# Kernel optimization log

Measured on AMD Instinct MI355X. Metric: run time of the kernel, lower is better.

The kernel has to match this reference:

```python
import jax, jax.numpy as jnp
import numpy as np

EPS = 0.1  # residual scale from __init__


def setup_inputs() -> dict:
    key = jax.random.key(0)
    ks = jax.random.split(key, 13)
    T, B, E = 8, 4096, 16          # terms, batch(queries), predicates(edges)
    F = 1024                        # feature_dim = 2*emb_dim (emb_dim=512)
    M = 2 * F + 2                   # message_dim = 4*emb_dim + 2 = 2050
    H = 4096                        # hidden_dim

    def lin(k, fan_in, shape):
        return jax.random.normal(k, shape, jnp.float32) / np.sqrt(fan_in)

    return {
        "term_emb": jax.random.normal(ks[0], (T, B, F), jnp.float32),
        "pred_emb": jax.random.normal(ks[1], (E, B, F), jnp.float32),
        "W1": lin(ks[2], M, (M, H)),
        "b1": jnp.zeros((H,), jnp.float32),
        "W2": lin(ks[3], H, (H, F)),
        "b2": jnp.zeros((F,), jnp.float32),
        "M1": lin(ks[4], F, (F, H)),
        "mb1": jnp.zeros((H,), jnp.float32),
        "M2": lin(ks[5], H, (H, F)),
        "mb2": jnp.zeros((F,), jnp.float32),
        "head_idx": jax.random.randint(ks[6], (E,), 0, T, jnp.int32),
        "tail_idx": jax.random.randint(ks[7], (E,), 0, T, jnp.int32),
        "sign_bits": jax.random.randint(ks[8], (E,), 0, 2, jnp.int32),
    }


def reference(term_emb, pred_emb, W1, b1, W2, b2, M1, mb1, M2, mb2,
              head_idx, tail_idx, sign_bits):
    # term_emb: [T,B,F], pred_emb: [E,B,F]
    T = term_emb.shape[0]
    E, B, F = pred_emb.shape
    dt = pred_emb.dtype

    sign = (1.0 - 2.0 * sign_bits.astype(dt))[:, None, None]   # [E,1,1], +-1
    ones = jnp.ones((E, B, 1), dt)
    s_ones = sign * ones                                        # [E,B,1]

    h = term_emb[head_idx]                                      # gather [E,B,F]
    t = term_emb[tail_idx]                                      # gather [E,B,F]

    # message to head: [head_emb, pred_emb, +1, sign]
    # message to tail: [tail_emb, pred_emb, -1, sign]
    msg_h = jnp.concatenate([h, pred_emb, ones, s_ones], axis=-1)   # [E,B,M]
    msg_t = jnp.concatenate([t, pred_emb, -ones, s_ones], axis=-1)  # [E,B,M]

    msgs = jnp.concatenate([msg_h, msg_t], axis=0)              # [2E,B,M]
    seg = jnp.concatenate([head_idx, tail_idx], axis=0)         # [2E]
    agg = jax.ops.segment_sum(msgs, seg, num_segments=T)        # [T,B,M]

    # encoder MLP + eps residual
    enc = jax.nn.relu(agg @ W1 + b1) @ W2 + b2                  # [T,B,F]
    x = enc + EPS * term_emb

    # update MLP (layers == 1)
    out = jax.nn.relu(x @ M1 + mb1) @ M2 + mb2                  # [T,B,F]
    return out
```

## Files before the change

kernel.cpp:

```cpp
#include <hip/hip_runtime.h>
#include <hip/hip_bf16.h>
#include <cstdint>

typedef unsigned short u16;
typedef __attribute__((ext_vector_type(8))) u16 u16x8;
typedef __attribute__((ext_vector_type(8))) short s16x8;
typedef __attribute__((ext_vector_type(4))) float f32x4;

#define AS1(p) ((const __attribute__((address_space(1))) void*)(p))
#define AS3(p) ((__attribute__((address_space(3))) void*)(p))

__device__ __forceinline__ u16 f2bf(float f){
  union{float f; uint32_t i;} x; x.f = f;
  uint32_t r = x.i + 0x7fff + ((x.i>>16)&1);
  return (u16)(r>>16);
}

__global__ void transpose_f32_bf16(const float* __restrict__ in, u16* __restrict__ out,
                                   int K, int N){
  __shared__ u16 tile[32][33];
  const int tid = threadIdx.x;
  const int bx = blockIdx.x, by = blockIdx.y;
  const int xl = tid & 31, yl = tid >> 5;
  #pragma unroll
  for (int r = 0; r < 4; ++r){
    int y = by*32 + yl + r*8;
    tile[yl + r*8][xl] = f2bf(in[(size_t)y*N + bx*32 + xl]);
  }
  __syncthreads();
  #pragma unroll
  for (int r = 0; r < 4; ++r){
    int oy = bx*32 + yl + r*8;
    int ox = by*32 + xl;
    out[(size_t)oy*K + ox] = tile[xl][yl + r*8];
  }
}

__global__ void build_bias1(const float* __restrict__ W1, const float* __restrict__ b1,
                            const int* __restrict__ head, const int* __restrict__ tail,
                            const int* __restrict__ sign, float* __restrict__ bias1){
  int idx = blockIdx.x*256 + threadIdx.x;
  int t = idx >> 12, h = idx & 4095;
  float cH = 0.f, cS = 0.f;
  #pragma unroll
  for (int e = 0; e < 16; ++e){
    float s = 1.f - 2.f*(float)sign[e];
    if (head[e] == t){ cH += 1.f; cS += s; }
    if (tail[e] == t){ cH -= 1.f; cS += s; }
  }
  bias1[idx] = b1[h] + cH*W1[(size_t)2048*4096 + h] + cS*W1[(size_t)2049*4096 + h];
}

__global__ void build_x1(const float* __restrict__ term, const float* __restrict__ pred,
                         const int* __restrict__ head, const int* __restrict__ tail,
                         u16* __restrict__ X1, int r0){
  int idx = blockIdx.x*256 + threadIdx.x;
  int lr = idx >> 8;
  int c8 = (idx & 255) * 8;
  int grow = r0 + lr;
  int t = grow >> 12;
  int b = grow & 4095;
  float v[8];
  if (c8 < 1024){
    int deg = 0;
    #pragma unroll
    for (int e = 0; e < 16; ++e) deg += (head[e]==t) + (tail[e]==t);
    float d = (float)deg;
    const float4* p = (const float4*)(term + (size_t)grow*1024 + c8);
    float4 lo = p[0], hi = p[1];
    v[0]=d*lo.x; v[1]=d*lo.y; v[2]=d*lo.z; v[3]=d*lo.w;
    v[4]=d*hi.x; v[5]=d*hi.y; v[6]=d*hi.z; v[7]=d*hi.w;
  } else {
    int f = c8 - 1024;
    #pragma unroll
    for (int j = 0; j < 8; ++j) v[j] = 0.f;
    #pragma unroll
    for (int e = 0; e < 16; ++e){
      int w = (head[e]==t) + (tail[e]==t);
      if (w){
        const float4* p = (const float4*)(pred + ((size_t)e<<22) + ((size_t)b<<10) + f);
        float4 lo = p[0], hi = p[1];
        float fw = (float)w;
        v[0]+=fw*lo.x; v[1]+=fw*lo.y; v[2]+=fw*lo.z; v[3]+=fw*lo.w;
        v[4]+=fw*hi.x; v[5]+=fw*hi.y; v[6]+=fw*hi.z; v[7]+=fw*hi.w;
      }
    }
  }
  u16x8 o;
  #pragma unroll
  for (int j = 0; j < 8; ++j) o[j] = f2bf(v[j]);
  *(u16x8*)(X1 + (size_t)lr*2048 + c8) = o;
}

#define FENCE() asm volatile("" ::: "memory")
#define BAR()   do{ FENCE(); __builtin_amdgcn_s_barrier(); FENCE(); }while(0)
#define LGKM0() do{ asm volatile("s_waitcnt lgkmcnt(0)" ::: "memory"); \
                    __builtin_amdgcn_sched_barrier(0); }while(0)
#define VM6()   asm volatile("s_waitcnt vmcnt(6)" ::: "memory")

#define STAGE(isB, slot, half, kt) do{ \
    const u16* _s = (isB ? bStage : aStage) + ((half) ? halfStride : (size_t)0) + ((size_t)(kt) << 6); \
    u16* _d = &LDS[(isB ? 32768 : 0) + (slot)*16384 + (half)*8192 + tid*8]; \
    __builtin_amdgcn_global_load_lds(AS1(_s), AS3(_d), 16, 0, 0); \
    __builtin_amdgcn_global_load_lds(AS1(_s + q2s), AS3(_d + 4096), 16, 0, 0); \
  }while(0)

#define LOADA(slot, rh) do{ \
    _Pragma("unroll") \
    for (int ii = 0; ii < 4; ++ii){ \
      af[ii][0] = *(const s16x8*)&LDS[(slot)*16384 + aB + ((rh)*4+ii)*1024 + xv0]; \
      af[ii][1] = *(const s16x8*)&LDS[(slot)*16384 + aB + ((rh)*4+ii)*1024 + xv1]; \
    } }while(0)

#define LOADB(slot) do{ \
    _Pragma("unroll") \
    for (int jj = 0; jj < 4; ++jj){ \
      bfr[jj][0] = *(const s16x8*)&LDS[32768 + (slot)*16384 + bB + jj*1024 + xv0]; \
      bfr[jj][1] = *(const s16x8*)&LDS[32768 + (slot)*16384 + bB + jj*1024 + xv1]; \
    } }while(0)

#define MFMAQ(rh, ch) do{ \
    _Pragma("unroll") \
    for (int ii = 0; ii < 4; ++ii){ \
      _Pragma("unroll") \
      for (int jj = 0; jj < 2; ++jj){ \
        acc[(rh)*4+ii][(ch)*2+jj] = __builtin_amdgcn_mfma_f32_16x16x32_bf16(af[ii][0], bfr[(ch)*2+jj][0], acc[(rh)*4+ii][(ch)*2+jj], 0,0,0); \
        acc[(rh)*4+ii][(ch)*2+jj] = __builtin_amdgcn_mfma_f32_16x16x32_bf16(af[ii][1], bfr[(ch)*2+jj][1], acc[(rh)*4+ii][(ch)*2+jj], 0,0,0); \
      } } }while(0)

template<int MODE>
__launch_bounds__(512, 2)
__global__ void gemm256(const u16* __restrict__ A, const u16* __restrict__ Bt,
                        void* __restrict__ Cv, int N, int K, int r0,
                        const float* __restrict__ bias_mat,
                        const float* __restrict__ bias_vec,
                        const float* __restrict__ resid){
  __shared__ u16 LDS[65536];
  const int tid = threadIdx.x;
  const int lane = tid & 63;
  const int wid = tid >> 6;
  const int wr = wid >> 2, wc = wid & 3;
  const int frow = lane & 15, fgrp = lane >> 4;

  int nwg = gridDim.x * gridDim.y;
  int orig = blockIdx.y * gridDim.x + blockIdx.x;
  int id = orig;
  if ((nwg & 7) == 0){ int cpx = nwg >> 3; id = (orig & 7) * cpx + (orig >> 3); }
  const int bx = id % gridDim.x, by = id / gridDim.x;
  const int row0 = by * 256, col0 = bx * 256;

  const size_t rowK = (size_t)(tid >> 3) * K;
  const int sg8 = (((tid & 7) ^ ((tid >> 3) & 7)) << 3);
  const u16* aStage = A  + (size_t)row0 * K + rowK + sg8;
  const u16* bStage = Bt + (size_t)col0 * K + rowK + sg8;
  const size_t halfStride = (size_t)128 * K;
  const size_t q2s = (size_t)64 * K;

  const int xv0 = ((fgrp)     ^ (frow & 7)) << 3;
  const int xv1 = ((4 + fgrp) ^ (frow & 7)) << 3;
  const int aB = wr * 8192 + frow * 64;
  const int bB = (wc >> 1) * 8192 + (wc & 1) * 4096 + frow * 64;

  f32x4 acc[8][4];
  #pragma unroll
  for (int i = 0; i < 8; ++i)
    #pragma unroll
    for (int j = 0; j < 4; ++j) acc[i][j] = (f32x4){0.f,0.f,0.f,0.f};
  s16x8 af[4][2], bfr[4][2];

  const int NT = K >> 6;
  const int NI = NT >> 1;

  STAGE(1,0,0,0); STAGE(1,0,1,0); STAGE(0,0,0,0); STAGE(0,0,1,0);
  STAGE(1,1,0,1); STAGE(1,1,1,1); STAGE(0,1,0,1);
  VM6(); BAR();

  for (int i = 0; i < NI; ++i){
    const int kt1  = 2*i + 1;
    const int kn0  = (2*i + 2 < NT) ? 2*i + 2 : NT - 2;
    const int kn1  = (2*i + 3 < NT) ? 2*i + 3 : NT - 1;
    LOADA(0,0); LOADB(0);
    STAGE(0,1,1,kt1);
    BAR(); LGKM0();
    __builtin_amdgcn_s_setprio(1); MFMAQ(0,0); __builtin_amdgcn_s_setprio(0);
    BAR();
    STAGE(1,0,0,kn0);
    BAR();
    __builtin_amdgcn_s_setprio(1); MFMAQ(0,1); __builtin_amdgcn_s_setprio(0);
    BAR();
    LOADA(0,1);
    STAGE(1,0,1,kn0);
    BAR(); LGKM0();
    __builtin_amdgcn_s_setprio(1); MFMAQ(1,0); __builtin_amdgcn_s_setprio(0);
    BAR();
    STAGE(0,0,0,kn0);
    BAR();
    __builtin_amdgcn_s_setprio(1); MFMAQ(1,1); __builtin_amdgcn_s_setprio(0);
    VM6(); BAR();
    LOADA(1,0); LOADB(1);
    STAGE(0,0,1,kn0);
    BAR(); LGKM0();
    __builtin_amdgcn_s_setprio(1); MFMAQ(0,0); __builtin_amdgcn_s_setprio(0);
    BAR();
    STAGE(1,1,0,kn1);
    BAR();
    __builtin_amdgcn_s_setprio(1); MFMAQ(0,1); __builtin_amdgcn_s_setprio(0);
    BAR();
    LOADA(1,1);
    STAGE(1,1,1,kn1);
    BAR(); LGKM0();
    __builtin_amdgcn_s_setprio(1); MFMAQ(1,0); __builtin_amdgcn_s_setprio(0);
    BAR();
    STAGE(0,1,0,kn1);
    BAR();
    __builtin_amdgcn_s_setprio(1); MFMAQ(1,1); __builtin_amdgcn_s_setprio(0);
    VM6(); BAR();
  }

  #pragma unroll
  for (int i2 = 0; i2 < 8; ++i2){
    #pragma unroll
    for (int j2 = 0; j2 < 4; ++j2){
      #pragma unroll
      for (int r = 0; r < 4; ++r){
        int lrow = row0 + wr*128 + i2*16 + fgrp*4 + r;
        int col  = col0 + wc*64 + j2*16 + frow;
        float v = acc[i2][j2][r];
        if (MODE == 0){
          int grow = r0 + lrow;
          v += bias_mat[(size_t)(grow >> 12)*N + col];
          v = fmaxf(v, 0.f);
          ((u16*)Cv)[(size_t)lrow*N + col] = f2bf(v);
        } else if (MODE == 1){
          int grow = r0 + lrow;
          v += bias_vec[col] + 0.1f*resid[(size_t)grow*1024 + col];
          ((u16*)Cv)[(size_t)lrow*N + col] = f2bf(v);
        } else if (MODE == 2){
          v += bias_vec[col];
          v = fmaxf(v, 0.f);
          ((u16*)Cv)[(size_t)lrow*N + col] = f2bf(v);
        } else {
          v += bias_vec[col];
          ((float*)Cv)[(size_t)lrow*N + col] = v;
        }
      }
    }
  }
}

extern "C" void kernel_launch(void* const* d_in, const int* in_sizes, int n_in,
                              void* d_out, int out_size, void* d_ws, size_t ws_size,
                              hipStream_t stream){
  const float* term = (const float*)d_in[0];
  const float* pred = (const float*)d_in[1];
  const float* W1   = (const float*)d_in[2];
  const float* b1   = (const float*)d_in[3];
  const float* W2   = (const float*)d_in[4];
  const float* b2   = (const float*)d_in[5];
  const float* M1   = (const float*)d_in[6];
  const float* mb1  = (const float*)d_in[7];
  const float* M2   = (const float*)d_in[8];
  const float* mb2  = (const float*)d_in[9];
  const int* head = (const int*)d_in[10];
  const int* tail = (const int*)d_in[11];
  const int* sign = (const int*)d_in[12];
  float* out = (float*)d_out;

  char* ws = (char*)d_ws;
  u16* W1T = (u16*)ws;  ws += (size_t)4096*2048*2;
  u16* W2T = (u16*)ws;  ws += (size_t)1024*4096*2;
  u16* M1T = (u16*)ws;  ws += (size_t)4096*1024*2;
  u16* M2T = (u16*)ws;  ws += (size_t)1024*4096*2;
  float* bias1 = (float*)ws; ws += (size_t)8*4096*4;
  size_t used = (size_t)(ws - (char*)d_ws);

  int R = 32768;
  while (R > 256 && used + (size_t)R*12288 > ws_size) R >>= 1;
  u16* bufA = (u16*)ws;
  u16* bufB = (u16*)(ws + (size_t)R*2048*2);

  transpose_f32_bf16<<<dim3(4096/32, 2048/32), 256, 0, stream>>>(W1, W1T, 2048, 4096);
  transpose_f32_bf16<<<dim3(1024/32, 4096/32), 256, 0, stream>>>(W2, W2T, 4096, 1024);
  transpose_f32_bf16<<<dim3(4096/32, 1024/32), 256, 0, stream>>>(M1, M1T, 1024, 4096);
  transpose_f32_bf16<<<dim3(1024/32, 4096/32), 256, 0, stream>>>(M2, M2T, 4096, 1024);
  build_bias1<<<dim3(8*4096/256), 256, 0, stream>>>(W1, b1, head, tail, sign, bias1);

  for (int r0 = 0; r0 < 32768; r0 += R){
    build_x1<<<dim3(R), 256, 0, stream>>>(term, pred, head, tail, bufA, r0);
    gemm256<0><<<dim3(4096/256, R/256), 512, 0, stream>>>(bufA, W1T, bufB, 4096, 2048, r0, bias1, nullptr, nullptr);
    gemm256<1><<<dim3(1024/256, R/256), 512, 0, stream>>>(bufB, W2T, bufA, 1024, 4096, r0, nullptr, b2, term);
    gemm256<2><<<dim3(4096/256, R/256), 512, 0, stream>>>(bufA, M1T, bufB, 4096, 1024, r0, nullptr, mb1, nullptr);
    gemm256<3><<<dim3(1024/256, R/256), 512, 0, stream>>>(bufB, M2T, out + (size_t)r0*1024, 1024, 4096, r0, nullptr, mb2, nullptr);
  }
}
```

Before: 1.352 ms.

## Reschedule GEMM main loop with split B fragment loads and new staging order

```diff
diff --git a/kernel.cpp b/kernel.cpp
--- a/kernel.cpp
+++ b/kernel.cpp
@@ -96,7 +96,8 @@
 #define BAR()   do{ FENCE(); __builtin_amdgcn_s_barrier(); FENCE(); }while(0)
 #define LGKM0() do{ asm volatile("s_waitcnt lgkmcnt(0)" ::: "memory"); \
                     __builtin_amdgcn_sched_barrier(0); }while(0)
-#define VM6()   asm volatile("s_waitcnt vmcnt(6)" ::: "memory")
+#define LGKM8() asm volatile("s_waitcnt lgkmcnt(8)" ::: "memory")
+#define VM4()   asm volatile("s_waitcnt vmcnt(4)" ::: "memory")
 
 #define STAGE(isB, slot, half, kt) do{ \
     const u16* _s = (isB ? bStage : aStage) + ((half) ? halfStride : (size_t)0) + ((size_t)(kt) << 6); \
@@ -112,9 +113,16 @@
       af[ii][1] = *(const s16x8*)&LDS[(slot)*16384 + aB + ((rh)*4+ii)*1024 + xv1]; \
     } }while(0)
 
-#define LOADB(slot) do{ \
+#define LOADB01(slot) do{ \
     _Pragma("unroll") \
-    for (int jj = 0; jj < 4; ++jj){ \
+    for (int jj = 0; jj < 2; ++jj){ \
+      bfr[jj][0] = *(const s16x8*)&LDS[32768 + (slot)*16384 + bB + jj*1024 + xv0]; \
+      bfr[jj][1] = *(const s16x8*)&LDS[32768 + (slot)*16384 + bB + jj*1024 + xv1]; \
+    } }while(0)
+
+#define LOADB23(slot) do{ \
+    _Pragma("unroll") \
+    for (int jj = 2; jj < 4; ++jj){ \
       bfr[jj][0] = *(const s16x8*)&LDS[32768 + (slot)*16384 + bB + jj*1024 + xv0]; \
       bfr[jj][1] = *(const s16x8*)&LDS[32768 + (slot)*16384 + bB + jj*1024 + xv1]; \
     } }while(0)
@@ -127,6 +135,9 @@
         acc[(rh)*4+ii][(ch)*2+jj] = __builtin_amdgcn_mfma_f32_16x16x32_bf16(af[ii][0], bfr[(ch)*2+jj][0], acc[(rh)*4+ii][(ch)*2+jj], 0,0,0); \
         acc[(rh)*4+ii][(ch)*2+jj] = __builtin_amdgcn_mfma_f32_16x16x32_bf16(af[ii][1], bfr[(ch)*2+jj][1], acc[(rh)*4+ii][(ch)*2+jj], 0,0,0); \
       } } }while(0)
+
+#define PRIO_MFMA(rh, ch) do{ \
+    __builtin_amdgcn_s_setprio(1); MFMAQ(rh, ch); __builtin_amdgcn_s_setprio(0); }while(0)
 
 template<int MODE>
 __launch_bounds__(512, 2)
@@ -172,49 +183,53 @@
   const int NI = NT >> 1;
 
   STAGE(1,0,0,0); STAGE(1,0,1,0); STAGE(0,0,0,0); STAGE(0,0,1,0);
-  STAGE(1,1,0,1); STAGE(1,1,1,1); STAGE(0,1,0,1);
-  VM6(); BAR();
+  STAGE(1,1,0,1); STAGE(1,1,1,1);
+  VM4(); BAR();
 
   for (int i = 0; i < NI; ++i){
-    const int kt1  = 2*i + 1;
-    const int kn0  = (2*i + 2 < NT) ? 2*i + 2 : NT - 2;
-    const int kn1  = (2*i + 3 < NT) ? 2*i + 3 : NT - 1;
-    LOADA(0,0); LOADB(0);
+    const int kt1 = 2*i + 1;
+    const int kn0 = (2*i + 2 < NT) ? 2*i + 2 : NT - 2;
+    const int kn1 = (2*i + 3 < NT) ? 2*i + 3 : NT - 1;
+    LOADA(0,0); LOADB01(0);
+    STAGE(0,1,0,kt1);
+    LGKM8();
+    BAR(); LGKM0();
+    PRIO_MFMA(0,0);
+    BAR();
+    LOADB23(0);
     STAGE(0,1,1,kt1);
     BAR(); LGKM0();
-    __builtin_amdgcn_s_setprio(1); MFMAQ(0,0); __builtin_amdgcn_s_setprio(0);
-    BAR();
+    PRIO_MFMA(0,1);
+    BAR();
+    LOADA(0,1);
     STAGE(1,0,0,kn0);
-    BAR();
-    __builtin_amdgcn_s_setprio(1); MFMAQ(0,1); __builtin_amdgcn_s_setprio(0);
-    BAR();
-    LOADA(0,1);
+    BAR(); LGKM0();
+    PRIO_MFMA(1,1);
+    BAR();
     STAGE(1,0,1,kn0);
-    BAR(); LGKM0();
-    __builtin_amdgcn_s_setprio(1); MFMAQ(1,0); __builtin_amdgcn_s_setprio(0);
-    BAR();
+    BAR();
+    PRIO_MFMA(1,0);
+    VM4(); BAR();
+    LOADA(1,0); LOADB01(1);
     STAGE(0,0,0,kn0);
-    BAR();
-    __builtin_amdgcn_s_setprio(1); MFMAQ(1,1); __builtin_amdgcn_s_setprio(0);
-    VM6(); BAR();
-    LOADA(1,0); LOADB(1);
+    LGKM8();
+    BAR(); LGKM0();
+    PRIO_MFMA(0,0);
+    BAR();
+    LOADB23(1);
     STAGE(0,0,1,kn0);
     BAR(); LGKM0();
-    __builtin_amdgcn_s_setprio(1); MFMAQ(0,0); __builtin_amdgcn_s_setprio(0);
-    BAR();
+    PRIO_MFMA(0,1);
+    BAR();
+    LOADA(1,1);
     STAGE(1,1,0,kn1);
-    BAR();
-    __builtin_amdgcn_s_setprio(1); MFMAQ(0,1); __builtin_amdgcn_s_setprio(0);
-    BAR();
-    LOADA(1,1);
+    BAR(); LGKM0();
+    PRIO_MFMA(1,1);
+    BAR();
     STAGE(1,1,1,kn1);
-    BAR(); LGKM0();
-    __builtin_amdgcn_s_setprio(1); MFMAQ(1,0); __builtin_amdgcn_s_setprio(0);
-    BAR();
-    STAGE(0,1,0,kn1);
-    BAR();
-    __builtin_amdgcn_s_setprio(1); MFMAQ(1,1); __builtin_amdgcn_s_setprio(0);
-    VM6(); BAR();
+    BAR();
+    PRIO_MFMA(1,0);
+    VM4(); BAR();
   }
 
   #pragma unroll
```

Measured after the change: 1.342 ms. About the same (-0.8%).
